# Kernel optimization log

Hardware: AMD Instinct MI355X
Metric: run time of the kernel (lower is better)

The kernel has to match this reference:

```python
import jax, jax.numpy as jnp
import numpy as np

N = 50000
E = 800000
IN_C, HID_C, OUT_C = 128, 256, 2


def sage_conv(x, src, dst, W_l, b_l, W_r, num_nodes):
    # PyG SAGEConv with mean aggregation:
    #   out = lin_l(mean_{j in N(i)} x_j) + lin_r(x_i)
    msg = x[src]                                            # [E, d] gather
    agg = jax.ops.segment_sum(msg, dst, num_segments=num_nodes)   # [N, d]
    cnt = jax.ops.segment_sum(jnp.ones((msg.shape[0],), x.dtype), dst,
                              num_segments=num_nodes)        # [N]
    agg = agg / jnp.maximum(cnt, 1.0)[:, None]               # mean (deg>=1)
    return agg @ W_l.T + b_l + x @ W_r.T


def setup_inputs() -> dict:
    key = jax.random.key(0)
    ks = jax.random.split(key, 8)
    x = jax.random.normal(ks[0], (N, IN_C), dtype=jnp.float32)
    edge_index = jax.random.randint(ks[1], (2, E), 0, N, dtype=jnp.int32)
    # glorot-ish scaled params
    s1 = 1.0 / np.sqrt(IN_C)
    s2 = 1.0 / np.sqrt(HID_C)
    W1l = jax.random.normal(ks[2], (HID_C, IN_C), dtype=jnp.float32) * s1
    W1r = jax.random.normal(ks[3], (HID_C, IN_C), dtype=jnp.float32) * s1
    b1 = jnp.zeros((HID_C,), dtype=jnp.float32)
    W2l = jax.random.normal(ks[4], (OUT_C, HID_C), dtype=jnp.float32) * s2
    W2r = jax.random.normal(ks[5], (OUT_C, HID_C), dtype=jnp.float32) * s2
    b2 = jnp.zeros((OUT_C,), dtype=jnp.float32)
    return {"x": x, "edge_index": edge_index,
            "W1l": W1l, "b1": b1, "W1r": W1r,
            "W2l": W2l, "b2": b2, "W2r": W2r}


def reference(x, edge_index, W1l, b1, W1r, W2l, b2, W2r):
    src, dst = edge_index[0], edge_index[1]
    h = sage_conv(x, src, dst, W1l, b1, W1r, N)
    h = jax.nn.relu(h)
    out = sage_conv(h, src, dst, W2l, b2, W2r, N)
    return out
```

## Files before the change

kernel.cpp:

```cpp
#include <hip/hip_runtime.h>
#include <hip/hip_bf16.h>


#define IN_C 128
#define HID_C 256
#define BKT_SHIFT 7
#define BKT_W 128
#define CAP 3072

typedef __attribute__((ext_vector_type(8))) short short8;
typedef __attribute__((ext_vector_type(4))) float f32x4;

static __device__ __forceinline__ unsigned short f2b(float f) {
    __hip_bfloat16 h = __float2bfloat16(f);
    return *(unsigned short*)&h;
}
static __device__ __forceinline__ float b2f(unsigned short u) {
    unsigned v = ((unsigned)u) << 16;
    return *(float*)&v;
}

__global__ __launch_bounds__(512) void scatter_conv(
    const float* __restrict__ x, unsigned int* __restrict__ Abf,
    const float* __restrict__ w1l, const float* __restrict__ w1r,
    unsigned short* __restrict__ Bg,
    const int* __restrict__ ei, int* __restrict__ bcnt,
    unsigned int* __restrict__ binned,
    int nquads , int xblk, int E_) {
    __shared__ int hist[512];
    __shared__ int lbase[512];
    const int tid = threadIdx.x;
    if (blockIdx.x < xblk) {
        int t = blockIdx.x * 512 + tid;
        if (t >= nquads) return;
        float4 v = *(const float4*)&x[(size_t)t * 4];
        uint2 o;
        o.x = ((unsigned)f2b(v.y) << 16) | f2b(v.x);
        o.y = ((unsigned)f2b(v.w) << 16) | f2b(v.z);
        int node = t >> 5, g = t & 31;
        *(uint2*)&Abf[(size_t)node * 128 + 64 + g * 2] = o;
    } else if (blockIdx.x < xblk + 32) {
        int idx4 = (blockIdx.x - xblk) * 512 + tid;
        int o = idx4 >> 6, k4 = (idx4 & 63) * 4;
        const float* srcp = (k4 < IN_C) ? &w1l[o * IN_C + k4]
                                        : &w1r[o * IN_C + (k4 - IN_C)];
        float4 f = *(const float4*)srcp;
        ushort4 s;
        s.x = f2b(f.x); s.y = f2b(f.y); s.z = f2b(f.z); s.w = f2b(f.w);
        *(ushort4*)&Bg[(size_t)idx4 * 4] = s;
    } else {
        const int e0 = (blockIdx.x - xblk - 32) * 2048;
        hist[tid] = 0;
        __syncthreads();
        int dreg[4];
#pragma unroll
        for (int j = 0; j < 4; ++j) {
            int e = e0 + j * 512 + tid;
            dreg[j] = (e < E_) ? ei[E_ + e] : -1;
            if (dreg[j] >= 0) atomicAdd(&hist[dreg[j] >> BKT_SHIFT], 1);
        }
        __syncthreads();
        {
            int c = hist[tid];
            lbase[tid] = c ? tid * CAP + atomicAdd(&bcnt[tid], c) : 0;
            hist[tid] = 0;
        }
        __syncthreads();
#pragma unroll
        for (int j = 0; j < 4; ++j) {
            int e = e0 + j * 512 + tid;
            if (dreg[j] >= 0) {
                int d = dreg[j];
                int b = d >> BKT_SHIFT;
                int pos = lbase[b] + atomicAdd(&hist[b], 1);
                if (pos < b * CAP + CAP)
                    binned[pos] = ((unsigned)ei[e] << BKT_SHIFT) |
                                  (unsigned)(d & (BKT_W - 1));
            }
        }
    }
}


__global__ __launch_bounds__(1024) void sort_gather(
    unsigned int* __restrict__ binned, const int* __restrict__ bcnt,
    const uint4* __restrict__ abf4c, uint4* __restrict__ Abf4,
    int* __restrict__ deg, int* __restrict__ boffs, int n) {
    __shared__ unsigned int ebuf[CAP];
    __shared__ unsigned short sbuf[CAP];
    __shared__ int hist[BKT_W];
    __shared__ int offs[BKT_W];
    __shared__ int cur[BKT_W];
    const int tid = threadIdx.x;
    const int lane = tid & 63;
    const int bkt = blockIdx.x;
    const int gbase = bkt * CAP;
    int cnt = bcnt[bkt];
    if (cnt > CAP) cnt = CAP;

    if (tid < BKT_W) hist[tid] = 0;
    {
        const int cnt4 = cnt >> 2;
        const uint4* b4 = (const uint4*)(binned + gbase);
        uint4* e4 = (uint4*)ebuf;
        for (int i = tid; i < cnt4; i += 1024) e4[i] = b4[i];
        for (int i = cnt4 * 4 + tid; i < cnt; i += 1024)
            ebuf[i] = binned[gbase + i];
    }
    __syncthreads();
    for (int i = tid; i < cnt; i += 1024)
        atomicAdd(&hist[ebuf[i] & (BKT_W - 1)], 1);
    __syncthreads();
    if (tid < 64) {
        int h0 = hist[lane * 2], h1 = hist[lane * 2 + 1];
        int s = h0 + h1;
        int incl = s;
#pragma unroll
        for (int off = 1; off < 64; off <<= 1) {
            int t = __shfl_up(incl, off);
            if (lane >= off) incl += t;
        }
        int excl = incl - s;
        offs[lane * 2] = excl;          cur[lane * 2] = excl;
        offs[lane * 2 + 1] = excl + h0; cur[lane * 2 + 1] = excl + h0;
    }
    __syncthreads();
    for (int i = tid; i < cnt; i += 1024) {
        unsigned int pk = ebuf[i];
        int pos = atomicAdd(&cur[pk & (BKT_W - 1)], 1);
        sbuf[pos] = (unsigned short)(pk >> BKT_SHIFT);
    }
    if (tid < BKT_W) {
        int node = bkt * BKT_W + tid;
        if (node < n) { deg[node] = hist[tid]; boffs[node] = offs[tid]; }
    }
    __syncthreads();

    {
        unsigned int* so = (unsigned int*)(binned + gbase);
        const int half = (cnt + 1) >> 1;
        for (int i = tid; i < half; i += 1024) {
            unsigned lo = sbuf[i * 2];
            unsigned hi = (i * 2 + 1 < cnt) ? sbuf[i * 2 + 1] : 0u;
            so[i] = lo | (hi << 16);
        }
    }

    const int wv = tid >> 6;
    const int ep = lane >> 4;
    const int pos = lane & 15;
    for (int ld = wv * 8; ld < wv * 8 + 8; ++ld) {
        int node = bkt * BKT_W + ld;
        if (node >= n) break;
        int beg = offs[ld], end = offs[ld] + hist[ld];
        float s[8] = {0.f, 0.f, 0.f, 0.f, 0.f, 0.f, 0.f, 0.f};
        for (int e = beg; e < end; e += 16) {
#pragma unroll
            for (int g = 0; g < 4; ++g) {
                int eg = e + g * 4 + ep;
                if (eg < end) {
                    int src = sbuf[eg];
                    uint4 u = abf4c[(size_t)src * 32 + 16 + pos];
                    s[0] += b2f(u.x & 0xffff); s[1] += b2f(u.x >> 16);
                    s[2] += b2f(u.y & 0xffff); s[3] += b2f(u.y >> 16);
                    s[4] += b2f(u.z & 0xffff); s[5] += b2f(u.z >> 16);
                    s[6] += b2f(u.w & 0xffff); s[7] += b2f(u.w >> 16);
                }
            }
        }
#pragma unroll
        for (int i = 0; i < 8; ++i) {
            s[i] += __shfl_xor(s[i], 16);
            s[i] += __shfl_xor(s[i], 32);
        }
        if (ep == 0) {
            float inv = 1.0f / (float)max(end - beg, 1);
            uint4 o;
            o.x = ((unsigned)f2b(s[1] * inv) << 16) | f2b(s[0] * inv);
            o.y = ((unsigned)f2b(s[3] * inv) << 16) | f2b(s[2] * inv);
            o.z = ((unsigned)f2b(s[5] * inv) << 16) | f2b(s[4] * inv);
            o.w = ((unsigned)f2b(s[7] * inv) << 16) | f2b(s[6] * inv);
            Abf4[(size_t)node * 32 + pos] = o;
        }
    }
}


__global__ __launch_bounds__(256, 4) void gemm1_fused(
    const unsigned short* __restrict__ Abf, const unsigned short* __restrict__ Bg,
    const float* __restrict__ b1, const float* __restrict__ w2l,
    const float* __restrict__ w2r, float* __restrict__ p2g,
    float* __restrict__ rsg, int nn) {
    const int tid = threadIdx.x;
    const int lane = tid & 63;
    const int wid = tid >> 6;
    const int wm = wid >> 1, wn = wid & 1;
    const int row0 = blockIdx.x * 128;
    const int col0 = blockIdx.y * 128;
    const int quad = lane >> 4;
    const int l16 = lane & 15;

    const unsigned short* ap[4];
#pragma unroll
    for (int mt = 0; mt < 4; ++mt) {
        int ar = row0 + wm * 64 + mt * 16 + l16;
        ap[mt] = Abf + (size_t)ar * 256 + quad * 8;
    }
    const unsigned short* bp[4];
#pragma unroll
    for (int nt = 0; nt < 4; ++nt) {
        int bc = col0 + wn * 64 + nt * 16 + l16;
        bp[nt] = Bg + (size_t)bc * 256 + quad * 8;
    }

    f32x4 acc[4][4];
#pragma unroll
    for (int i = 0; i < 4; ++i)
#pragma unroll
        for (int j = 0; j < 4; ++j) acc[i][j] = (f32x4){0.f, 0.f, 0.f, 0.f};

#pragma unroll 2
    for (int ks = 0; ks < 8; ++ks) {
        short8 af[4], bf[4];
#pragma unroll
        for (int mt = 0; mt < 4; ++mt)
            af[mt] = *(const short8*)(ap[mt] + ks * 32);
#pragma unroll
        for (int nt = 0; nt < 4; ++nt)
            bf[nt] = *(const short8*)(bp[nt] + ks * 32);
#pragma unroll
        for (int mt = 0; mt < 4; ++mt)
#pragma unroll
            for (int nt = 0; nt < 4; ++nt)
                acc[mt][nt] = __builtin_amdgcn_mfma_f32_16x16x32_bf16(
                    af[mt], bf[nt], acc[mt][nt], 0, 0, 0);
    }

    const int cbase = col0 + wn * 64 + l16;
#pragma unroll
    for (int half = 0; half < 2; ++half) {
        const float* wA = half ? w2r : w2l;
        float* og = half ? rsg : p2g;
        f32x4 part[2][4];
#pragma unroll
        for (int c = 0; c < 2; ++c)
#pragma unroll
            for (int mt = 0; mt < 4; ++mt) part[c][mt] = (f32x4){0.f, 0.f, 0.f, 0.f};
#pragma unroll
        for (int nt = 0; nt < 4; ++nt) {
            const int col = cbase + nt * 16;
            const float bias = b1[col];
            const float w0 = wA[col];
            const float w1 = wA[HID_C + col];
#pragma unroll
            for (int mt = 0; mt < 4; ++mt)
#pragma unroll
                for (int r = 0; r < 4; ++r) {
                    float hv = fmaxf(acc[mt][nt][r] + bias, 0.0f);
                    part[0][mt][r] += hv * w0;
                    part[1][mt][r] += hv * w1;
                }
        }
#pragma unroll
        for (int c = 0; c < 2; ++c)
#pragma unroll
            for (int mt = 0; mt < 4; ++mt)
#pragma unroll
                for (int r = 0; r < 4; ++r)
#pragma unroll
                    for (int m = 1; m < 16; m <<= 1)
                        part[c][mt][r] += __shfl_xor(part[c][mt][r], m);
        if (l16 < 8) {
            const int ch2 = l16 & 1;
            const int mts = l16 >> 1;
#pragma unroll
            for (int r = 0; r < 4; ++r) {
                int row = row0 + wm * 64 + quad * 4 + mts * 16 + r;
                if (row < nn)
                    atomicAdd(&og[row * 2 + ch2], part[ch2][mts][r]);
            }
        }
    }
}


__global__ __launch_bounds__(512) void fin_bucket(
    const unsigned int* __restrict__ binned, const int* __restrict__ boffs,
    const int* __restrict__ deg,
    const float2* __restrict__ p2, const float2* __restrict__ rs,
    const float* __restrict__ b2, float* __restrict__ out, int n) {
    __shared__ float ps0[3][BKT_W];
    __shared__ float ps1[3][BKT_W];
    const int tid = threadIdx.x;
    const int ln = tid & (BKT_W - 1);
    const int hp = tid >> 7;
    const int bkt = blockIdx.x;
    const int node = bkt * BKT_W + ln;
    const unsigned short* sp =
        (const unsigned short*)(binned + (size_t)bkt * CAP);
    float s0 = 0.f, s1 = 0.f;
    int dg = 0;
    if (node < n) {
        int beg = boffs[node];
        dg = deg[node];
        int end = beg + dg;
        for (int i = beg + hp; i < end; i += 4) {
            float2 v = p2[sp[i]];
            s0 += v.x; s1 += v.y;
        }
    }
    if (hp) { ps0[hp - 1][ln] = s0; ps1[hp - 1][ln] = s1; }
    __syncthreads();
    if (!hp && node < n) {
        s0 += ps0[0][ln] + ps0[1][ln] + ps0[2][ln];
        s1 += ps1[0][ln] + ps1[1][ln] + ps1[2][ln];
        float inv = 1.0f / (float)max(dg, 1);
        float2 self = rs[node];
        out[node * 2 + 0] = s0 * inv + self.x + b2[0];
        out[node * 2 + 1] = s1 * inv + self.y + b2[1];
    }
}


extern "C" void kernel_launch(void* const* d_in, const int* in_sizes, int n_in,
                              void* d_out, int out_size, void* d_ws, size_t ws_size,
                              hipStream_t stream) {
    const float* x   = (const float*)d_in[0];
    const int*   ei  = (const int*)d_in[1];
    const float* W1l = (const float*)d_in[2];
    const float* b1  = (const float*)d_in[3];
    const float* W1r = (const float*)d_in[4];
    const float* W2l = (const float*)d_in[5];
    const float* b2  = (const float*)d_in[6];
    const float* W2r = (const float*)d_in[7];
    float* out = (float*)d_out;

    const int N_ = in_sizes[0] / IN_C;
    const int E_ = in_sizes[1] / 2;
    const int nbkt = (N_ + BKT_W - 1) / BKT_W;

    char* wsb = (char*)d_ws;
    size_t off = 0;
    auto alloc = [&](size_t bytes) {
        void* ptr = wsb + off;
        off += ((bytes + 15) & ~(size_t)15);
        return ptr;
    };
    unsigned short* Abf = (unsigned short*)alloc((size_t)N_ * 256 * 2);
    unsigned short* Bg  = (unsigned short*)alloc(256 * 256 * 2);
    unsigned int* binned = (unsigned int*)alloc((size_t)(nbkt + 1) * CAP * 4);
    int*   bcnt = (int*)alloc(512 * 4);
    float* p2f  = (float*)alloc((size_t)N_ * 2 * 4);
    float* rsf  = (float*)alloc((size_t)N_ * 2 * 4);
    int*   deg  = (int*)alloc((size_t)N_ * 4);
    int*   boffs = (int*)alloc((size_t)N_ * 4);

    const int xblk = (N_ * 32 + 511) / 512;
    const int eblk = (E_ + 2047) / 2048;

    hipMemsetAsync(bcnt, 0, 512 * sizeof(int) + (size_t)N_ * 2 * 4 * 2, stream);

    scatter_conv<<<xblk + 32 + eblk, 512, 0, stream>>>(
        x, (unsigned int*)Abf, W1l, W1r, Bg, ei, bcnt, binned,
        N_ * 32, xblk, E_);

    sort_gather<<<nbkt, 1024, 0, stream>>>(binned, bcnt, (const uint4*)Abf,
                                           (uint4*)Abf, deg, boffs, N_);

    gemm1_fused<<<dim3((N_ + 127) / 128, 2), 256, 0, stream>>>(
        Abf, Bg, b1, W2l, W2r, p2f, rsf, N_);

    fin_bucket<<<nbkt, 512, 0, stream>>>(binned, boffs, deg,
                                         (const float2*)p2f, (const float2*)rsf,
                                         b2, out, N_);
}
```

Measured before the change: 209.6 us.

## Restructure GEMM1 to full-width column tiles with LDS-staged weights and local reduction

The fused first-layer GEMM now gives each block 64 rows across all 256 hidden columns instead of a 128x128 tile on a 2D grid. The weight matrix is staged through padded shared memory in 64-wide K chunks, and the layer-2 projection partials are reduced in shared memory and written once per row. This removes the global atomics and the memset of the p2/rs buffers, and each A row is read by only one block. In exchange, every block reloads the full B matrix through LDS with extra barriers, and there are more, smaller blocks.

```diff
diff --git a/kernel.cpp b/kernel.cpp
--- a/kernel.cpp
+++ b/kernel.cpp
@@ -186,32 +186,29 @@
 }
 
 
+#define LSTR 72
+
 __global__ __launch_bounds__(256, 4) void gemm1_fused(
     const unsigned short* __restrict__ Abf, const unsigned short* __restrict__ Bg,
     const float* __restrict__ b1, const float* __restrict__ w2l,
-    const float* __restrict__ w2r, float* __restrict__ p2g,
-    float* __restrict__ rsg, int nn) {
+    const float* __restrict__ w2r, float2* __restrict__ p2g,
+    float2* __restrict__ rsg, int nn) {
+    __shared__ short Bs[256 * LSTR];
+
     const int tid = threadIdx.x;
     const int lane = tid & 63;
-    const int wid = tid >> 6;
-    const int wm = wid >> 1, wn = wid & 1;
-    const int row0 = blockIdx.x * 128;
-    const int col0 = blockIdx.y * 128;
+    const int wn = tid >> 6;
+    const int row0 = blockIdx.x * 64;
     const int quad = lane >> 4;
     const int l16 = lane & 15;
 
     const unsigned short* ap[4];
 #pragma unroll
     for (int mt = 0; mt < 4; ++mt) {
-        int ar = row0 + wm * 64 + mt * 16 + l16;
+        int ar = row0 + mt * 16 + l16;
+        if (ar >= nn) ar = nn - 1;
         ap[mt] = Abf + (size_t)ar * 256 + quad * 8;
     }
-    const unsigned short* bp[4];
-#pragma unroll
-    for (int nt = 0; nt < 4; ++nt) {
-        int bc = col0 + wn * 64 + nt * 16 + l16;
-        bp[nt] = Bg + (size_t)bc * 256 + quad * 8;
-    }
 
     f32x4 acc[4][4];
 #pragma unroll
@@ -219,28 +216,43 @@
 #pragma unroll
         for (int j = 0; j < 4; ++j) acc[i][j] = (f32x4){0.f, 0.f, 0.f, 0.f};
 
-#pragma unroll 2
-    for (int ks = 0; ks < 8; ++ks) {
-        short8 af[4], bf[4];
-#pragma unroll
-        for (int mt = 0; mt < 4; ++mt)
-            af[mt] = *(const short8*)(ap[mt] + ks * 32);
-#pragma unroll
-        for (int nt = 0; nt < 4; ++nt)
-            bf[nt] = *(const short8*)(bp[nt] + ks * 32);
-#pragma unroll
-        for (int mt = 0; mt < 4; ++mt)
+    for (int k0 = 0; k0 < 256; k0 += 64) {
+        const uint4* gb = (const uint4*)(Bg + (size_t)tid * 256 + k0);
+        uint4 r0 = gb[0], r1 = gb[1], r2 = gb[2], r3 = gb[3];
+        uint4 r4 = gb[4], r5 = gb[5], r6 = gb[6], r7 = gb[7];
+        __syncthreads();
+        uint4* lb = (uint4*)&Bs[tid * LSTR];
+        lb[0] = r0; lb[1] = r1; lb[2] = r2; lb[3] = r3;
+        lb[4] = r4; lb[5] = r5; lb[6] = r6; lb[7] = r7;
+        __syncthreads();
+
+#pragma unroll
+        for (int kb = 0; kb < 2; ++kb) {
+            short8 af[4], bf[4];
+#pragma unroll
+            for (int mt = 0; mt < 4; ++mt)
+                af[mt] = *(const short8*)(ap[mt] + k0 + kb * 32);
 #pragma unroll
             for (int nt = 0; nt < 4; ++nt)
-                acc[mt][nt] = __builtin_amdgcn_mfma_f32_16x16x32_bf16(
-                    af[mt], bf[nt], acc[mt][nt], 0, 0, 0);
-    }
-
-    const int cbase = col0 + wn * 64 + l16;
+                bf[nt] = *(const short8*)&Bs[(wn * 64 + nt * 16 + l16) * LSTR + kb * 32 + quad * 8];
+#pragma unroll
+            for (int mt = 0; mt < 4; ++mt)
+#pragma unroll
+                for (int nt = 0; nt < 4; ++nt)
+                    acc[mt][nt] = __builtin_amdgcn_mfma_f32_16x16x32_bf16(
+                        af[mt], bf[nt], acc[mt][nt], 0, 0, 0);
+        }
+    }
+
+    float* pr = (float*)Bs;
+    __syncthreads();
+    pr[tid] = 0.f;
+    __syncthreads();
+
+    const int cbase = wn * 64 + l16;
 #pragma unroll
     for (int half = 0; half < 2; ++half) {
         const float* wA = half ? w2r : w2l;
-        float* og = half ? rsg : p2g;
         f32x4 part[2][4];
 #pragma unroll
         for (int c = 0; c < 2; ++c)
@@ -275,10 +287,19 @@
             const int mts = l16 >> 1;
 #pragma unroll
             for (int r = 0; r < 4; ++r) {
-                int row = row0 + wm * 64 + quad * 4 + mts * 16 + r;
-                if (row < nn)
-                    atomicAdd(&og[row * 2 + ch2], part[ch2][mts][r]);
+                int rloc = quad * 4 + mts * 16 + r;
+                atomicAdd(&pr[rloc * 4 + half * 2 + ch2], part[ch2][mts][r]);
             }
+        }
+    }
+    __syncthreads();
+    if (tid < 128) {
+        int rloc = tid >> 1, pair = tid & 1;
+        int row = row0 + rloc;
+        if (row < nn) {
+            float2 v = make_float2(pr[rloc * 4 + pair * 2],
+                                   pr[rloc * 4 + pair * 2 + 1]);
+            if (pair) rsg[row] = v; else p2g[row] = v;
         }
     }
 }
@@ -358,7 +379,7 @@
     const int xblk = (N_ * 32 + 511) / 512;
     const int eblk = (E_ + 2047) / 2048;
 
-    hipMemsetAsync(bcnt, 0, 512 * sizeof(int) + (size_t)N_ * 2 * 4 * 2, stream);
+    hipMemsetAsync(bcnt, 0, 512 * sizeof(int), stream);
 
     scatter_conv<<<xblk + 32 + eblk, 512, 0, stream>>>(
         x, (unsigned int*)Abf, W1l, W1r, Bg, ei, bcnt, binned,
@@ -367,8 +388,8 @@
     sort_gather<<<nbkt, 1024, 0, stream>>>(binned, bcnt, (const uint4*)Abf,
                                            (uint4*)Abf, deg, boffs, N_);
 
-    gemm1_fused<<<dim3((N_ + 127) / 128, 2), 256, 0, stream>>>(
-        Abf, Bg, b1, W2l, W2r, p2f, rsf, N_);
+    gemm1_fused<<<(N_ + 63) / 64, 256, 0, stream>>>(
+        Abf, Bg, b1, W2l, W2r, (float2*)p2f, (float2*)rsf, N_);
 
     fin_bucket<<<nbkt, 512, 0, stream>>>(binned, boffs, deg,
                                          (const float2*)p2f, (const float2*)rsf,
```

After: 213.6 us. About the same (+1.9%).
